# Kernel optimization log

Hardware: AMD Instinct MI355X
Metric: run time of the kernel (lower is better)

The kernel has to match this reference:

```python
import jax, jax.numpy as jnp
import numpy as np

BATCH, DIN, DSTATE, SEQLEN = 4, 2048, 16, 2048


def setup_inputs() -> dict:
    key = jax.random.key(0)
    ks = jax.random.split(key, 7)
    u = jax.random.normal(ks[0], (BATCH, DIN, SEQLEN), dtype=jnp.float32)
    # delta pre-softplus; moderate positive-ish values like Mamba dt_proj output
    delta = jax.random.uniform(ks[1], (BATCH, DIN, SEQLEN), dtype=jnp.float32, minval=-2.0, maxval=1.0)
    # A is negative in real Mamba (A = -exp(A_log)); keep recurrence stable
    A = -jnp.exp(jax.random.uniform(ks[2], (DIN, DSTATE), dtype=jnp.float32, minval=-1.0, maxval=1.0))
    B = jax.random.normal(ks[3], (BATCH, DSTATE, SEQLEN), dtype=jnp.float32)
    C = jax.random.normal(ks[4], (BATCH, DSTATE, SEQLEN), dtype=jnp.float32)
    D = jax.random.normal(ks[5], (DIN,), dtype=jnp.float32)
    z = jax.random.normal(ks[6], (BATCH, DIN, SEQLEN), dtype=jnp.float32)
    return {"u": u, "delta": delta, "A": A, "B": B, "C": C, "D": D, "z": z}


def reference(u, delta, A, B, C, D, z):
    """Mamba selective scan (selective_scan_ref semantics, delta_softplus=True).

    u, delta, z: (b, d, l); A: (d, n); B, C: (b, n, l); D: (d,).
    y_t = C_t . x_t + D*u_t, x_t = exp(dt_t*A)*x_{t-1} + dt_t*B_t*u_t,
    final y gated by SiLU(z).
    """
    dt = jax.nn.softplus(delta)                      # (b, d, l)

    def step(x, inp):
        dt_t, u_t, B_t, C_t = inp                    # (b,d) (b,d) (b,n) (b,n)
        dA = jnp.exp(dt_t[..., None] * A)            # (b, d, n)
        x = x * dA + (dt_t * u_t)[..., None] * B_t[:, None, :]
        y_t = jnp.einsum('bdn,bn->bd', x, C_t)
        return x, y_t

    xs = (jnp.moveaxis(dt, -1, 0),                   # (l, b, d)
          jnp.moveaxis(u, -1, 0),
          jnp.moveaxis(B, -1, 0),                    # (l, b, n)
          jnp.moveaxis(C, -1, 0))
    x0 = jnp.zeros((u.shape[0], u.shape[1], A.shape[1]), dtype=u.dtype)
    _, ys = jax.lax.scan(step, x0, xs)               # ys: (l, b, d)
    y = jnp.moveaxis(ys, 0, -1)                      # (b, d, l)
    y = y + D[None, :, None] * u
    y = y * (z * jax.nn.sigmoid(z))                  # SiLU gate
    return y
```

## Files before the change

### kernel.cpp

```cpp
#include <hip/hip_runtime.h>


#define BATCHSZ 4
#define DIN 2048
#define NSTATE 16
#define SEQ 2048
#define NCH (BATCHSZ * DIN)
#define TT 32
#define L2E 1.44269504f

__device__ __forceinline__ float softplus_f(float v) {
    float e = __builtin_amdgcn_exp2f(v * L2E);
    return 0.69314718f * __builtin_amdgcn_logf(1.0f + e);
}

__device__ __forceinline__ float silu_f(float v) {
    float s = __builtin_amdgcn_rcpf(1.0f + __builtin_amdgcn_exp2f(-v * L2E));
    return v * s;
}

__device__ __forceinline__ float comp4(const float4& f, int k) {
    return k == 0 ? f.x : k == 1 ? f.y : k == 2 ? f.z : f.w;
}

__device__ __forceinline__ void set4(float4& f, int k, float v) {
    if (k == 0) f.x = v; else if (k == 1) f.y = v; else if (k == 2) f.z = v; else f.w = v;
}


template<int NC>
__global__ __launch_bounds__(256, 3) void k_pass1(
        const float* __restrict__ u, const float* __restrict__ delta,
        const float* __restrict__ A, const float* __restrict__ Bm,
        float* __restrict__ ws) {
    constexpr int LC = SEQ / NC;
    constexpr int DB = DIN / 256;
    int blk = blockIdx.x;
    int b = (blk / DB) % BATCHSZ;
    int c = blk / (DB * BATCHSZ);
    int d = (blk % DB) * 256 + threadIdx.x;
    int bd = b * DIN + d;

    float A2[NSTATE];
    const float* Ar = A + d * NSTATE;
    #pragma unroll
    for (int n = 0; n < NSTATE; ++n) A2[n] = Ar[n] * L2E;

    float x[NSTATE];
    #pragma unroll
    for (int n = 0; n < NSTATE; ++n) x[n] = 0.0f;
    float S = 0.0f;

    size_t base = (size_t)bd * SEQ + (size_t)c * LC;
    const float4* u4 = (const float4*)(u + base);
    const float4* d4 = (const float4*)(delta + base);
    const float* Bp = Bm + (size_t)b * NSTATE * SEQ + (size_t)c * LC;

    for (int tile = 0; tile < LC / TT; ++tile) {
        float4 ub[8], db[8];
        #pragma unroll
        for (int j = 0; j < 8; ++j) { ub[j] = u4[tile * 8 + j]; db[j] = d4[tile * 8 + j]; }
        #pragma unroll
        for (int j = 0; j < 8; ++j) {
            #pragma unroll
            for (int k = 0; k < 4; ++k) {
                float dt = softplus_f(comp4(db[j], k));
                S += dt;
                float du = dt * comp4(ub[j], k);
                int t = tile * TT + j * 4 + k;
                #pragma unroll
                for (int n = 0; n < NSTATE; ++n) {
                    float dA = __builtin_amdgcn_exp2f(A2[n] * dt);
                    x[n] = x[n] * dA + du * Bp[n * SEQ + t];
                }
            }
        }
    }
    float* wsq = ws;
    float* wsS = ws + (size_t)NSTATE * NC * NCH;
    #pragma unroll
    for (int n = 0; n < NSTATE; ++n) wsq[((size_t)n * NC + c) * NCH + bd] = x[n];
    wsS[(size_t)c * NCH + bd] = S;
}

template<int NC>
__global__ __launch_bounds__(256) void k_pass2(
        const float* __restrict__ A, float* __restrict__ ws) {
    int bd = blockIdx.x * 256 + threadIdx.x;
    int d = bd & (DIN - 1);

    float A2[NSTATE];
    const float* Ar = A + d * NSTATE;
    #pragma unroll
    for (int n = 0; n < NSTATE; ++n) A2[n] = Ar[n] * L2E;

    float x[NSTATE];
    #pragma unroll
    for (int n = 0; n < NSTATE; ++n) x[n] = 0.0f;

    float* wsq = ws;
    float* wsS = ws + (size_t)NSTATE * NC * NCH;

    for (int c = 0; c < NC; ++c) {
        float S = wsS[(size_t)c * NCH + bd];
        #pragma unroll
        for (int n = 0; n < NSTATE; ++n) {
            float* p = wsq + ((size_t)n * NC + c) * NCH + bd;
            float q = *p;
            float P = __builtin_amdgcn_exp2f(A2[n] * S);
            *p = x[n];
            x[n] = x[n] * P + q;
        }
    }
}

template<int NC>
__global__ __launch_bounds__(256, 3) void k_pass3(
        const float* __restrict__ u, const float* __restrict__ delta,
        const float* __restrict__ A, const float* __restrict__ Bm,
        const float* __restrict__ Cm, const float* __restrict__ Dv,
        const float* __restrict__ z, const float* __restrict__ ws,
        float* __restrict__ out) {
    constexpr int LC = SEQ / NC;
    constexpr int DB = DIN / 256;
    int blk = blockIdx.x;
    int b = (blk / DB) % BATCHSZ;
    int c = blk / (DB * BATCHSZ);
    int d = (blk % DB) * 256 + threadIdx.x;
    int bd = b * DIN + d;

    float A2[NSTATE];
    const float* Ar = A + d * NSTATE;
    #pragma unroll
    for (int n = 0; n < NSTATE; ++n) A2[n] = Ar[n] * L2E;

    const float* wsq = ws;
    float x[NSTATE];
    #pragma unroll
    for (int n = 0; n < NSTATE; ++n)
        x[n] = wsq[((size_t)n * NC + c) * NCH + bd];

    float Dd = Dv[d];
    size_t base = (size_t)bd * SEQ + (size_t)c * LC;
    const float4* u4 = (const float4*)(u + base);
    const float4* d4 = (const float4*)(delta + base);
    const float4* z4 = (const float4*)(z + base);
    float4* o4 = (float4*)(out + base);
    const float* Bp = Bm + (size_t)b * NSTATE * SEQ + (size_t)c * LC;
    const float* Cp = Cm + (size_t)b * NSTATE * SEQ + (size_t)c * LC;

    for (int tile = 0; tile < LC / TT; ++tile) {
        float4 ub[8], db[8];
        #pragma unroll
        for (int j = 0; j < 8; ++j) { ub[j] = u4[tile * 8 + j]; db[j] = d4[tile * 8 + j]; }
        float4 yy[8];
        #pragma unroll
        for (int j = 0; j < 8; ++j) {
            #pragma unroll
            for (int k = 0; k < 4; ++k) {
                float uv = comp4(ub[j], k);
                float dt = softplus_f(comp4(db[j], k));
                float du = dt * uv;
                int t = tile * TT + j * 4 + k;
                float acc = 0.0f;
                #pragma unroll
                for (int n = 0; n < NSTATE; ++n) {
                    float dA = __builtin_amdgcn_exp2f(A2[n] * dt);
                    x[n] = x[n] * dA + du * Bp[n * SEQ + t];
                    acc += x[n] * Cp[n * SEQ + t];
                }
                set4(yy[j], k, acc + Dd * uv);
            }
        }
        float4 zb[8];
        #pragma unroll
        for (int j = 0; j < 8; ++j) zb[j] = z4[tile * 8 + j];
        #pragma unroll
        for (int j = 0; j < 8; ++j) {
            float4 oo;
            #pragma unroll
            for (int k = 0; k < 4; ++k)
                set4(oo, k, comp4(yy[j], k) * silu_f(comp4(zb[j], k)));
            o4[tile * 8 + j] = oo;
        }
    }
}

__global__ __launch_bounds__(256) void k_simple(
        const float* __restrict__ u, const float* __restrict__ delta,
        const float* __restrict__ A, const float* __restrict__ Bm,
        const float* __restrict__ Cm, const float* __restrict__ Dv,
        const float* __restrict__ z, float* __restrict__ out) {
    int bd = blockIdx.x * 256 + threadIdx.x;
    int b  = bd >> 11;
    int d  = bd & (DIN - 1);

    float A2[NSTATE];
    const float* Ar = A + d * NSTATE;
    #pragma unroll
    for (int n = 0; n < NSTATE; ++n) A2[n] = Ar[n] * L2E;
    float x[NSTATE];
    #pragma unroll
    for (int n = 0; n < NSTATE; ++n) x[n] = 0.0f;

    float Dd = Dv[d];
    size_t base = (size_t)bd * SEQ;
    const float4* u4 = (const float4*)(u + base);
    const float4* d4 = (const float4*)(delta + base);
    const float4* z4 = (const float4*)(z + base);
    float4* o4 = (float4*)(out + base);
    const float* Bp = Bm + (size_t)b * NSTATE * SEQ;
    const float* Cp = Cm + (size_t)b * NSTATE * SEQ;

    for (int t4 = 0; t4 < SEQ / 4; ++t4) {
        float4 uu = u4[t4];
        float4 dd = d4[t4];
        float4 zz = z4[t4];
        float4 yy;
        #pragma unroll
        for (int k = 0; k < 4; ++k) {
            float uv = comp4(uu, k);
            float dt = softplus_f(comp4(dd, k));
            float du = dt * uv;
            int t = t4 * 4 + k;
            float acc = 0.0f;
            #pragma unroll
            for (int n = 0; n < NSTATE; ++n) {
                float dA = __builtin_amdgcn_exp2f(A2[n] * dt);
                x[n] = x[n] * dA + du * Bp[n * SEQ + t];
                acc += x[n] * Cp[n * SEQ + t];
            }
            float y = acc + Dd * uv;
            y = y * silu_f(comp4(zz, k));
            set4(yy, k, y);
        }
        o4[t4] = yy;
    }
}

template<int NC>
static void launch_chunked(const float* u, const float* delta, const float* A,
                           const float* Bm, const float* Cm, const float* Dv,
                           const float* z, float* ws, float* out, hipStream_t stream) {
    k_pass1<NC><<<NCH * NC / 256, 256, 0, stream>>>(u, delta, A, Bm, ws);
    k_pass2<NC><<<NCH / 256, 256, 0, stream>>>(A, ws);
    k_pass3<NC><<<NCH * NC / 256, 256, 0, stream>>>(u, delta, A, Bm, Cm, Dv, z, ws, out);
}

extern "C" void kernel_launch(void* const* d_in, const int* in_sizes, int n_in,
                              void* d_out, int out_size, void* d_ws, size_t ws_size,
                              hipStream_t stream) {
    const float* u     = (const float*)d_in[0];
    const float* delta = (const float*)d_in[1];
    const float* A     = (const float*)d_in[2];
    const float* Bm    = (const float*)d_in[3];
    const float* Cm    = (const float*)d_in[4];
    const float* Dv    = (const float*)d_in[5];
    const float* z     = (const float*)d_in[6];
    float* out = (float*)d_out;
    float* ws = (float*)d_ws;

    size_t need32 = (size_t)(NSTATE + 1) * 32 * NCH * sizeof(float);
    size_t need16 = (size_t)(NSTATE + 1) * 16 * NCH * sizeof(float);
    if (ws_size >= need32) {
        launch_chunked<32>(u, delta, A, Bm, Cm, Dv, z, ws, out, stream);
    } else if (ws_size >= need16) {
        launch_chunked<16>(u, delta, A, Bm, Cm, Dv, z, ws, out, stream);
    } else {
        k_simple<<<NCH / 256, 256, 0, stream>>>(u, delta, A, Bm, Cm, Dv, z, out);
    }
}
```

Measured before the change: 459.9 us.

## Stage u/delta and B/C through LDS with coalesced loads, parallelize pass2 per state

Pass1 and pass3 now load u and delta tiles cooperatively with coalesced float4 reads into padded shared memory, prefetching the next tile into registers. The per-chunk B and C slices are transposed into shared memory so each timestep reads 16 states as four float4 LDS loads. Pass3 also writes y back through LDS so z reads and output stores are coalesced. Pass2 gets one thread per (state, channel) for more parallelism, and a 64-chunk variant is added when the workspace allows it. The cost is more shared memory, extra barriers, and lower occupancy.

```diff
diff --git a/kernel.cpp b/kernel.cpp
--- a/kernel.cpp
+++ b/kernel.cpp
@@ -6,7 +6,9 @@
 #define NSTATE 16
 #define SEQ 2048
 #define NCH (BATCHSZ * DIN)
-#define TT 32
+#define NGRP (NCH / 256)
+#define TT 16
+#define ST 20
 #define L2E 1.44269504f
 
 __device__ __forceinline__ float softplus_f(float v) {
@@ -34,48 +36,92 @@
         const float* __restrict__ A, const float* __restrict__ Bm,
         float* __restrict__ ws) {
     constexpr int LC = SEQ / NC;
-    constexpr int DB = DIN / 256;
-    int blk = blockIdx.x;
-    int b = (blk / DB) % BATCHSZ;
-    int c = blk / (DB * BATCHSZ);
-    int d = (blk % DB) * 256 + threadIdx.x;
-    int bd = b * DIN + d;
+    constexpr int NT = LC / TT;
+    __shared__ float Ub[256 * ST];
+    __shared__ float Db[256 * ST];
+    __shared__ float Bc[LC * 20];
+
+    int tid = threadIdx.x;
+    int g = blockIdx.x & (NGRP - 1);
+    int c = blockIdx.x >> 5;
+    int chBase = g << 8;
+    int b = chBase >> 11;
+    int bd = chBase + tid;
+    int d = bd & (DIN - 1);
 
     float A2[NSTATE];
-    const float* Ar = A + d * NSTATE;
-    #pragma unroll
-    for (int n = 0; n < NSTATE; ++n) A2[n] = Ar[n] * L2E;
+    {
+        const float* Ar = A + (size_t)d * NSTATE;
+        #pragma unroll
+        for (int n = 0; n < NSTATE; ++n) A2[n] = Ar[n] * L2E;
+    }
+
+    const float* ug = u + (size_t)chBase * SEQ + (size_t)c * LC;
+    const float* dg = delta + (size_t)chBase * SEQ + (size_t)c * LC;
+    const float* Bg = Bm + (size_t)b * NSTATE * SEQ + (size_t)c * LC;
+
+    #pragma unroll
+    for (int i = 0; i < LC * NSTATE / 256; ++i) {
+        int e = i * 256 + tid;
+        int n = e / LC;
+        int t = e % LC;
+        Bc[t * 20 + n] = Bg[(size_t)n * SEQ + t];
+    }
 
     float x[NSTATE];
     #pragma unroll
     for (int n = 0; n < NSTATE; ++n) x[n] = 0.0f;
     float S = 0.0f;
 
-    size_t base = (size_t)bd * SEQ + (size_t)c * LC;
-    const float4* u4 = (const float4*)(u + base);
-    const float4* d4 = (const float4*)(delta + base);
-    const float* Bp = Bm + (size_t)b * NSTATE * SEQ + (size_t)c * LC;
-
-    for (int tile = 0; tile < LC / TT; ++tile) {
-        float4 ub[8], db[8];
-        #pragma unroll
-        for (int j = 0; j < 8; ++j) { ub[j] = u4[tile * 8 + j]; db[j] = d4[tile * 8 + j]; }
-        #pragma unroll
-        for (int j = 0; j < 8; ++j) {
+    float4 uvr[4], dvr[4];
+    #pragma unroll
+    for (int it = 0; it < 4; ++it) {
+        int r = it * 64 + (tid >> 2), cq = (tid & 3) * 4;
+        uvr[it] = *(const float4*)(ug + (size_t)r * SEQ + cq);
+        dvr[it] = *(const float4*)(dg + (size_t)r * SEQ + cq);
+    }
+
+    for (int tile = 0; tile < NT; ++tile) {
+        int tb = tile * TT;
+        __syncthreads();
+        #pragma unroll
+        for (int it = 0; it < 4; ++it) {
+            int r = it * 64 + (tid >> 2), cq = (tid & 3) * 4;
+            *(float4*)(&Ub[r * ST + cq]) = uvr[it];
+            *(float4*)(&Db[r * ST + cq]) = dvr[it];
+        }
+        __syncthreads();
+        if (tile + 1 < NT) {
+            #pragma unroll
+            for (int it = 0; it < 4; ++it) {
+                int r = it * 64 + (tid >> 2), cq = (tid & 3) * 4;
+                uvr[it] = *(const float4*)(ug + (size_t)r * SEQ + tb + TT + cq);
+                dvr[it] = *(const float4*)(dg + (size_t)r * SEQ + tb + TT + cq);
+            }
+        }
+        #pragma unroll
+        for (int t4 = 0; t4 < TT / 4; ++t4) {
+            float4 u4 = *(const float4*)(&Ub[tid * ST + t4 * 4]);
+            float4 d4 = *(const float4*)(&Db[tid * ST + t4 * 4]);
             #pragma unroll
             for (int k = 0; k < 4; ++k) {
-                float dt = softplus_f(comp4(db[j], k));
+                float dt = softplus_f(comp4(d4, k));
                 S += dt;
-                float du = dt * comp4(ub[j], k);
-                int t = tile * TT + j * 4 + k;
+                float du = dt * comp4(u4, k);
+                int t = tb + t4 * 4 + k;
+                const float4* Br = (const float4*)(&Bc[t * 20]);
+                float bb[NSTATE];
+                *(float4*)&bb[0] = Br[0]; *(float4*)&bb[4] = Br[1];
+                *(float4*)&bb[8] = Br[2]; *(float4*)&bb[12] = Br[3];
                 #pragma unroll
                 for (int n = 0; n < NSTATE; ++n) {
                     float dA = __builtin_amdgcn_exp2f(A2[n] * dt);
-                    x[n] = x[n] * dA + du * Bp[n * SEQ + t];
+                    x[n] = x[n] * dA + du * bb[n];
                 }
             }
         }
     }
+
     float* wsq = ws;
     float* wsS = ws + (size_t)NSTATE * NC * NCH;
     #pragma unroll
@@ -86,31 +132,23 @@
 template<int NC>
 __global__ __launch_bounds__(256) void k_pass2(
         const float* __restrict__ A, float* __restrict__ ws) {
-    int bd = blockIdx.x * 256 + threadIdx.x;
+    int idx = blockIdx.x * 256 + threadIdx.x;
+    int n = idx >> 13;
+    int bd = idx & (NCH - 1);
     int d = bd & (DIN - 1);
 
-    float A2[NSTATE];
-    const float* Ar = A + d * NSTATE;
-    #pragma unroll
-    for (int n = 0; n < NSTATE; ++n) A2[n] = Ar[n] * L2E;
-
-    float x[NSTATE];
-    #pragma unroll
-    for (int n = 0; n < NSTATE; ++n) x[n] = 0.0f;
-
+    float A2 = A[(size_t)d * NSTATE + n] * L2E;
+    float x = 0.0f;
     float* wsq = ws;
     float* wsS = ws + (size_t)NSTATE * NC * NCH;
 
     for (int c = 0; c < NC; ++c) {
         float S = wsS[(size_t)c * NCH + bd];
-        #pragma unroll
-        for (int n = 0; n < NSTATE; ++n) {
-            float* p = wsq + ((size_t)n * NC + c) * NCH + bd;
-            float q = *p;
-            float P = __builtin_amdgcn_exp2f(A2[n] * S);
-            *p = x[n];
-            x[n] = x[n] * P + q;
-        }
+        float* p = wsq + ((size_t)n * NC + c) * NCH + bd;
+        float q = *p;
+        float P = __builtin_amdgcn_exp2f(A2 * S);
+        *p = x;
+        x = x * P + q;
     }
 }
 
@@ -122,66 +160,116 @@
         const float* __restrict__ z, const float* __restrict__ ws,
         float* __restrict__ out) {
     constexpr int LC = SEQ / NC;
-    constexpr int DB = DIN / 256;
-    int blk = blockIdx.x;
-    int b = (blk / DB) % BATCHSZ;
-    int c = blk / (DB * BATCHSZ);
-    int d = (blk % DB) * 256 + threadIdx.x;
-    int bd = b * DIN + d;
+    constexpr int NT = LC / TT;
+    __shared__ float Ub[256 * ST];
+    __shared__ float Db[256 * ST];
+    __shared__ float Bc[LC * 20];
+    __shared__ float Cc[LC * 20];
+
+    int tid = threadIdx.x;
+    int g = blockIdx.x & (NGRP - 1);
+    int c = blockIdx.x >> 5;
+    int chBase = g << 8;
+    int b = chBase >> 11;
+    int bd = chBase + tid;
+    int d = bd & (DIN - 1);
 
     float A2[NSTATE];
-    const float* Ar = A + d * NSTATE;
-    #pragma unroll
-    for (int n = 0; n < NSTATE; ++n) A2[n] = Ar[n] * L2E;
+    {
+        const float* Ar = A + (size_t)d * NSTATE;
+        #pragma unroll
+        for (int n = 0; n < NSTATE; ++n) A2[n] = Ar[n] * L2E;
+    }
+
+    const float* ug = u + (size_t)chBase * SEQ + (size_t)c * LC;
+    const float* dg = delta + (size_t)chBase * SEQ + (size_t)c * LC;
+    const float* zg = z + (size_t)chBase * SEQ + (size_t)c * LC;
+    float* og = out + (size_t)chBase * SEQ + (size_t)c * LC;
+    const float* Bg = Bm + (size_t)b * NSTATE * SEQ + (size_t)c * LC;
+    const float* Cg = Cm + (size_t)b * NSTATE * SEQ + (size_t)c * LC;
+
+    #pragma unroll
+    for (int i = 0; i < LC * NSTATE / 256; ++i) {
+        int e = i * 256 + tid;
+        int n = e / LC;
+        int t = e % LC;
+        Bc[t * 20 + n] = Bg[(size_t)n * SEQ + t];
+        Cc[t * 20 + n] = Cg[(size_t)n * SEQ + t];
+    }
 
     const float* wsq = ws;
     float x[NSTATE];
     #pragma unroll
     for (int n = 0; n < NSTATE; ++n)
         x[n] = wsq[((size_t)n * NC + c) * NCH + bd];
-
     float Dd = Dv[d];
-    size_t base = (size_t)bd * SEQ + (size_t)c * LC;
-    const float4* u4 = (const float4*)(u + base);
-    const float4* d4 = (const float4*)(delta + base);
-    const float4* z4 = (const float4*)(z + base);
-    float4* o4 = (float4*)(out + base);
-    const float* Bp = Bm + (size_t)b * NSTATE * SEQ + (size_t)c * LC;
-    const float* Cp = Cm + (size_t)b * NSTATE * SEQ + (size_t)c * LC;
-
-    for (int tile = 0; tile < LC / TT; ++tile) {
-        float4 ub[8], db[8];
-        #pragma unroll
-        for (int j = 0; j < 8; ++j) { ub[j] = u4[tile * 8 + j]; db[j] = d4[tile * 8 + j]; }
-        float4 yy[8];
-        #pragma unroll
-        for (int j = 0; j < 8; ++j) {
+
+    float4 uvr[4], dvr[4];
+    #pragma unroll
+    for (int it = 0; it < 4; ++it) {
+        int r = it * 64 + (tid >> 2), cq = (tid & 3) * 4;
+        uvr[it] = *(const float4*)(ug + (size_t)r * SEQ + cq);
+        dvr[it] = *(const float4*)(dg + (size_t)r * SEQ + cq);
+    }
+
+    for (int tile = 0; tile < NT; ++tile) {
+        int tb = tile * TT;
+        __syncthreads();
+        #pragma unroll
+        for (int it = 0; it < 4; ++it) {
+            int r = it * 64 + (tid >> 2), cq = (tid & 3) * 4;
+            *(float4*)(&Ub[r * ST + cq]) = uvr[it];
+            *(float4*)(&Db[r * ST + cq]) = dvr[it];
+        }
+        __syncthreads();
+        if (tile + 1 < NT) {
+            #pragma unroll
+            for (int it = 0; it < 4; ++it) {
+                int r = it * 64 + (tid >> 2), cq = (tid & 3) * 4;
+                uvr[it] = *(const float4*)(ug + (size_t)r * SEQ + tb + TT + cq);
+                dvr[it] = *(const float4*)(dg + (size_t)r * SEQ + tb + TT + cq);
+            }
+        }
+        #pragma unroll
+        for (int t4 = 0; t4 < TT / 4; ++t4) {
+            float4 u4 = *(const float4*)(&Ub[tid * ST + t4 * 4]);
+            float4 d4 = *(const float4*)(&Db[tid * ST + t4 * 4]);
+            float4 y4;
             #pragma unroll
             for (int k = 0; k < 4; ++k) {
-                float uv = comp4(ub[j], k);
-                float dt = softplus_f(comp4(db[j], k));
+                float uv = comp4(u4, k);
+                float dt = softplus_f(comp4(d4, k));
                 float du = dt * uv;
-                int t = tile * TT + j * 4 + k;
+                int t = tb + t4 * 4 + k;
+                const float4* Br = (const float4*)(&Bc[t * 20]);
+                const float4* Cr = (const float4*)(&Cc[t * 20]);
+                float bb[NSTATE], cc[NSTATE];
+                *(float4*)&bb[0] = Br[0]; *(float4*)&bb[4] = Br[1];
+                *(float4*)&bb[8] = Br[2]; *(float4*)&bb[12] = Br[3];
+                *(float4*)&cc[0] = Cr[0]; *(float4*)&cc[4] = Cr[1];
+                *(float4*)&cc[8] = Cr[2]; *(float4*)&cc[12] = Cr[3];
                 float acc = 0.0f;
                 #pragma unroll
                 for (int n = 0; n < NSTATE; ++n) {
                     float dA = __builtin_amdgcn_exp2f(A2[n] * dt);
-                    x[n] = x[n] * dA + du * Bp[n * SEQ + t];
-                    acc += x[n] * Cp[n * SEQ + t];
+                    x[n] = x[n] * dA + du * bb[n];
+                    acc += x[n] * cc[n];
                 }
-                set4(yy[j], k, acc + Dd * uv);
-            }
-        }
-        float4 zb[8];
-        #pragma unroll
-        for (int j = 0; j < 8; ++j) zb[j] = z4[tile * 8 + j];
-        #pragma unroll
-        for (int j = 0; j < 8; ++j) {
+                set4(y4, k, acc + Dd * uv);
+            }
+            *(float4*)(&Ub[tid * ST + t4 * 4]) = y4;
+        }
+        __syncthreads();
+        #pragma unroll
+        for (int it = 0; it < 4; ++it) {
+            int r = it * 64 + (tid >> 2), cq = (tid & 3) * 4;
+            float4 y4 = *(const float4*)(&Ub[r * ST + cq]);
+            float4 z4 = *(const float4*)(zg + (size_t)r * SEQ + tb + cq);
             float4 oo;
             #pragma unroll
             for (int k = 0; k < 4; ++k)
-                set4(oo, k, comp4(yy[j], k) * silu_f(comp4(zb[j], k)));
-            o4[tile * 8 + j] = oo;
+                set4(oo, k, comp4(y4, k) * silu_f(comp4(z4, k)));
+            *(float4*)(og + (size_t)r * SEQ + tb + cq) = oo;
         }
     }
 }
@@ -242,9 +330,9 @@
 static void launch_chunked(const float* u, const float* delta, const float* A,
                            const float* Bm, const float* Cm, const float* Dv,
                            const float* z, float* ws, float* out, hipStream_t stream) {
-    k_pass1<NC><<<NCH * NC / 256, 256, 0, stream>>>(u, delta, A, Bm, ws);
-    k_pass2<NC><<<NCH / 256, 256, 0, stream>>>(A, ws);
-    k_pass3<NC><<<NCH * NC / 256, 256, 0, stream>>>(u, delta, A, Bm, Cm, Dv, z, ws, out);
+    k_pass1<NC><<<NGRP * NC, 256, 0, stream>>>(u, delta, A, Bm, ws);
+    k_pass2<NC><<<(NSTATE * NCH) / 256, 256, 0, stream>>>(A, ws);
+    k_pass3<NC><<<NGRP * NC, 256, 0, stream>>>(u, delta, A, Bm, Cm, Dv, z, ws, out);
 }
 
 extern "C" void kernel_launch(void* const* d_in, const int* in_sizes, int n_in,
@@ -260,9 +348,12 @@
     float* out = (float*)d_out;
     float* ws = (float*)d_ws;
 
+    size_t need64 = (size_t)(NSTATE + 1) * 64 * NCH * sizeof(float);
     size_t need32 = (size_t)(NSTATE + 1) * 32 * NCH * sizeof(float);
     size_t need16 = (size_t)(NSTATE + 1) * 16 * NCH * sizeof(float);
-    if (ws_size >= need32) {
+    if (ws_size >= need64) {
+        launch_chunked<64>(u, delta, A, Bm, Cm, Dv, z, ws, out, stream);
+    } else if (ws_size >= need32) {
         launch_chunked<32>(u, delta, A, Bm, Cm, Dv, z, ws, out, stream);
     } else if (ws_size >= need16) {
         launch_chunked<16>(u, delta, A, Bm, Cm, Dv, z, ws, out, stream);
```

Result: faster. 445.0 us (-3.3%).

## Restructure chunked scan into windowed segments with LDS-staged B/C and per-state pass2

Applied to the files above, without the earlier changes.

Rework the three-pass chunked scan so each block covers 32 channels across a 256-step window, with 8 threads per channel scanning 32-step segments (64 chunks total). B and C for the window are staged in shared memory with padded rows. The carry pass is parallelised over both channel and state index, with vectorised, prefetched workspace access. This exposes more parallelism in the sequential carry pass and shortens per-thread dependency chains. In exchange it needs roughly twice the workspace, and if the workspace is too small it falls back to the slow single-pass kernel.

```diff
diff --git a/kernel.cpp b/kernel.cpp
--- a/kernel.cpp
+++ b/kernel.cpp
@@ -6,8 +6,18 @@
 #define NSTATE 16
 #define SEQ 2048
 #define NCH (BATCHSZ * DIN)
-#define TT 32
+#define CHG 32
+#define SEGS 8
+#define SLEN 32
+#define WIN 256
+#define NWIN 8
+#define NCP 64
+#define NG2 256
 #define L2E 1.44269504f
+
+#define WSQ_N 524288
+#define WSQ_T 65536
+#define WSS_OFF 8388608
 
 __device__ __forceinline__ float softplus_f(float v) {
     float e = __builtin_amdgcn_exp2f(v * L2E);
@@ -27,162 +37,208 @@
     if (k == 0) f.x = v; else if (k == 1) f.y = v; else if (k == 2) f.z = v; else f.w = v;
 }
 
-
-template<int NC>
 __global__ __launch_bounds__(256, 3) void k_pass1(
         const float* __restrict__ u, const float* __restrict__ delta,
         const float* __restrict__ A, const float* __restrict__ Bm,
         float* __restrict__ ws) {
-    constexpr int LC = SEQ / NC;
-    constexpr int DB = DIN / 256;
-    int blk = blockIdx.x;
-    int b = (blk / DB) % BATCHSZ;
-    int c = blk / (DB * BATCHSZ);
-    int d = (blk % DB) * 256 + threadIdx.x;
-    int bd = b * DIN + d;
+    __shared__ float Bc[WIN * 20];
+
+    int tid = threadIdx.x;
+    int g = blockIdx.x & (NG2 - 1);
+    int tau = blockIdx.x >> 8;
+    int ch = tid >> 3, seg = tid & 7;
+    int bd = g * CHG + ch;
+    int d = bd & (DIN - 1);
+    int b = bd >> 11;
+
+    const float* up = u + (size_t)bd * SEQ + tau * WIN + seg * SLEN;
+    const float* dp = delta + (size_t)bd * SEQ + tau * WIN + seg * SLEN;
+    float4 uv[8], dv[8];
+    #pragma unroll
+    for (int j = 0; j < 8; ++j) { uv[j] = ((const float4*)up)[j]; dv[j] = ((const float4*)dp)[j]; }
+
+    const float* Bg = Bm + (size_t)b * NSTATE * SEQ + tau * WIN;
+    #pragma unroll
+    for (int m = 0; m < 4; ++m) {
+        float4 v;
+        v.x = Bg[(size_t)(m * 4 + 0) * SEQ + tid];
+        v.y = Bg[(size_t)(m * 4 + 1) * SEQ + tid];
+        v.z = Bg[(size_t)(m * 4 + 2) * SEQ + tid];
+        v.w = Bg[(size_t)(m * 4 + 3) * SEQ + tid];
+        *(float4*)(&Bc[tid * 20 + m * 4]) = v;
+    }
 
     float A2[NSTATE];
-    const float* Ar = A + d * NSTATE;
+    const float* Ar = A + (size_t)d * NSTATE;
     #pragma unroll
     for (int n = 0; n < NSTATE; ++n) A2[n] = Ar[n] * L2E;
+
+    __syncthreads();
 
     float x[NSTATE];
     #pragma unroll
     for (int n = 0; n < NSTATE; ++n) x[n] = 0.0f;
     float S = 0.0f;
 
-    size_t base = (size_t)bd * SEQ + (size_t)c * LC;
-    const float4* u4 = (const float4*)(u + base);
-    const float4* d4 = (const float4*)(delta + base);
-    const float* Bp = Bm + (size_t)b * NSTATE * SEQ + (size_t)c * LC;
-
-    for (int tile = 0; tile < LC / TT; ++tile) {
-        float4 ub[8], db[8];
-        #pragma unroll
-        for (int j = 0; j < 8; ++j) { ub[j] = u4[tile * 8 + j]; db[j] = d4[tile * 8 + j]; }
-        #pragma unroll
-        for (int j = 0; j < 8; ++j) {
+    #pragma unroll
+    for (int j = 0; j < 8; ++j) {
+        #pragma unroll
+        for (int k = 0; k < 4; ++k) {
+            float dt = softplus_f(comp4(dv[j], k));
+            S += dt;
+            float du = dt * comp4(uv[j], k);
+            int tl = seg * SLEN + j * 4 + k;
+            const float4* Br = (const float4*)(&Bc[tl * 20]);
+            float bb[NSTATE];
+            *(float4*)&bb[0] = Br[0]; *(float4*)&bb[4] = Br[1];
+            *(float4*)&bb[8] = Br[2]; *(float4*)&bb[12] = Br[3];
             #pragma unroll
-            for (int k = 0; k < 4; ++k) {
-                float dt = softplus_f(comp4(db[j], k));
-                S += dt;
-                float du = dt * comp4(ub[j], k);
-                int t = tile * TT + j * 4 + k;
-                #pragma unroll
-                for (int n = 0; n < NSTATE; ++n) {
-                    float dA = __builtin_amdgcn_exp2f(A2[n] * dt);
-                    x[n] = x[n] * dA + du * Bp[n * SEQ + t];
-                }
+            for (int n = 0; n < NSTATE; ++n) {
+                float dA = __builtin_amdgcn_exp2f(A2[n] * dt);
+                x[n] = x[n] * dA + du * bb[n];
             }
         }
     }
-    float* wsq = ws;
-    float* wsS = ws + (size_t)NSTATE * NC * NCH;
-    #pragma unroll
-    for (int n = 0; n < NSTATE; ++n) wsq[((size_t)n * NC + c) * NCH + bd] = x[n];
-    wsS[(size_t)c * NCH + bd] = S;
-}
-
-template<int NC>
+
+    size_t qb = (size_t)tau * WSQ_T + (size_t)g * 256 + ch * 8 + seg;
+    #pragma unroll
+    for (int n = 0; n < NSTATE; ++n) ws[(size_t)n * WSQ_N + qb] = x[n];
+    ws[WSS_OFF + qb] = S;
+}
+
 __global__ __launch_bounds__(256) void k_pass2(
         const float* __restrict__ A, float* __restrict__ ws) {
-    int bd = blockIdx.x * 256 + threadIdx.x;
+    int idx = blockIdx.x * 256 + threadIdx.x;
+    int n = idx >> 13;
+    int bd = idx & (NCH - 1);
+    int g = bd >> 5, ch = bd & 31;
     int d = bd & (DIN - 1);
 
-    float A2[NSTATE];
-    const float* Ar = A + d * NSTATE;
-    #pragma unroll
-    for (int n = 0; n < NSTATE; ++n) A2[n] = Ar[n] * L2E;
-
-    float x[NSTATE];
-    #pragma unroll
-    for (int n = 0; n < NSTATE; ++n) x[n] = 0.0f;
-
-    float* wsq = ws;
-    float* wsS = ws + (size_t)NSTATE * NC * NCH;
-
-    for (int c = 0; c < NC; ++c) {
-        float S = wsS[(size_t)c * NCH + bd];
-        #pragma unroll
-        for (int n = 0; n < NSTATE; ++n) {
-            float* p = wsq + ((size_t)n * NC + c) * NCH + bd;
-            float q = *p;
-            float P = __builtin_amdgcn_exp2f(A2[n] * S);
-            *p = x[n];
-            x[n] = x[n] * P + q;
-        }
-    }
-}
-
-template<int NC>
+    float A2 = A[(size_t)d * NSTATE + n] * L2E;
+
+    size_t qb = (size_t)n * WSQ_N + (size_t)g * 256 + ch * 8;
+    size_t sb = WSS_OFF + (size_t)g * 256 + ch * 8;
+
+    float x = 0.0f;
+    float4 Sa = *(const float4*)(ws + sb);
+    float4 Sb = *(const float4*)(ws + sb + 4);
+    float4 qa = *(const float4*)(ws + qb);
+    float4 q2 = *(const float4*)(ws + qb + 4);
+
+    #pragma unroll
+    for (int tau = 0; tau < NWIN; ++tau) {
+        float4 nSa, nSb, nqa, nq2;
+        if (tau + 1 < NWIN) {
+            nSa = *(const float4*)(ws + sb + (size_t)(tau + 1) * WSQ_T);
+            nSb = *(const float4*)(ws + sb + (size_t)(tau + 1) * WSQ_T + 4);
+            nqa = *(const float4*)(ws + qb + (size_t)(tau + 1) * WSQ_T);
+            nq2 = *(const float4*)(ws + qb + (size_t)(tau + 1) * WSQ_T + 4);
+        }
+        float Sv[8], qv[8], xs[8];
+        *(float4*)&Sv[0] = Sa; *(float4*)&Sv[4] = Sb;
+        *(float4*)&qv[0] = qa; *(float4*)&qv[4] = q2;
+        #pragma unroll
+        for (int s = 0; s < 8; ++s) {
+            xs[s] = x;
+            x = x * __builtin_amdgcn_exp2f(A2 * Sv[s]) + qv[s];
+        }
+        *(float4*)(ws + qb + (size_t)tau * WSQ_T) = *(float4*)&xs[0];
+        *(float4*)(ws + qb + (size_t)tau * WSQ_T + 4) = *(float4*)&xs[4];
+        Sa = nSa; Sb = nSb; qa = nqa; q2 = nq2;
+    }
+}
+
 __global__ __launch_bounds__(256, 3) void k_pass3(
         const float* __restrict__ u, const float* __restrict__ delta,
         const float* __restrict__ A, const float* __restrict__ Bm,
         const float* __restrict__ Cm, const float* __restrict__ Dv,
         const float* __restrict__ z, const float* __restrict__ ws,
         float* __restrict__ out) {
-    constexpr int LC = SEQ / NC;
-    constexpr int DB = DIN / 256;
-    int blk = blockIdx.x;
-    int b = (blk / DB) % BATCHSZ;
-    int c = blk / (DB * BATCHSZ);
-    int d = (blk % DB) * 256 + threadIdx.x;
-    int bd = b * DIN + d;
+    __shared__ float Bc[WIN * 20];
+    __shared__ float Cc[WIN * 20];
+
+    int tid = threadIdx.x;
+    int g = blockIdx.x & (NG2 - 1);
+    int tau = blockIdx.x >> 8;
+    int ch = tid >> 3, seg = tid & 7;
+    int bd = g * CHG + ch;
+    int d = bd & (DIN - 1);
+    int b = bd >> 11;
+
+    size_t qb = (size_t)tau * WSQ_T + (size_t)g * 256 + ch * 8 + seg;
+    float x[NSTATE];
+    #pragma unroll
+    for (int n = 0; n < NSTATE; ++n) x[n] = ws[(size_t)n * WSQ_N + qb];
+
+    const float* up = u + (size_t)bd * SEQ + tau * WIN + seg * SLEN;
+    const float* dp = delta + (size_t)bd * SEQ + tau * WIN + seg * SLEN;
+    float4 uv[8], dv[8];
+    #pragma unroll
+    for (int j = 0; j < 8; ++j) { uv[j] = ((const float4*)up)[j]; dv[j] = ((const float4*)dp)[j]; }
+
+    const float* Bg = Bm + (size_t)b * NSTATE * SEQ + tau * WIN;
+    const float* Cg = Cm + (size_t)b * NSTATE * SEQ + tau * WIN;
+    #pragma unroll
+    for (int m = 0; m < 4; ++m) {
+        float4 v, w;
+        v.x = Bg[(size_t)(m * 4 + 0) * SEQ + tid];
+        v.y = Bg[(size_t)(m * 4 + 1) * SEQ + tid];
+        v.z = Bg[(size_t)(m * 4 + 2) * SEQ + tid];
+        v.w = Bg[(size_t)(m * 4 + 3) * SEQ + tid];
+        w.x = Cg[(size_t)(m * 4 + 0) * SEQ + tid];
+        w.y = Cg[(size_t)(m * 4 + 1) * SEQ + tid];
+        w.z = Cg[(size_t)(m * 4 + 2) * SEQ + tid];
+        w.w = Cg[(size_t)(m * 4 + 3) * SEQ + tid];
+        *(float4*)(&Bc[tid * 20 + m * 4]) = v;
+        *(float4*)(&Cc[tid * 20 + m * 4]) = w;
+    }
 
     float A2[NSTATE];
-    const float* Ar = A + d * NSTATE;
+    const float* Ar = A + (size_t)d * NSTATE;
     #pragma unroll
     for (int n = 0; n < NSTATE; ++n) A2[n] = Ar[n] * L2E;
-
-    const float* wsq = ws;
-    float x[NSTATE];
-    #pragma unroll
-    for (int n = 0; n < NSTATE; ++n)
-        x[n] = wsq[((size_t)n * NC + c) * NCH + bd];
-
     float Dd = Dv[d];
-    size_t base = (size_t)bd * SEQ + (size_t)c * LC;
-    const float4* u4 = (const float4*)(u + base);
-    const float4* d4 = (const float4*)(delta + base);
-    const float4* z4 = (const float4*)(z + base);
-    float4* o4 = (float4*)(out + base);
-    const float* Bp = Bm + (size_t)b * NSTATE * SEQ + (size_t)c * LC;
-    const float* Cp = Cm + (size_t)b * NSTATE * SEQ + (size_t)c * LC;
-
-    for (int tile = 0; tile < LC / TT; ++tile) {
-        float4 ub[8], db[8];
-        #pragma unroll
-        for (int j = 0; j < 8; ++j) { ub[j] = u4[tile * 8 + j]; db[j] = d4[tile * 8 + j]; }
-        float4 yy[8];
-        #pragma unroll
-        for (int j = 0; j < 8; ++j) {
+
+    __syncthreads();
+
+    #pragma unroll
+    for (int j = 0; j < 8; ++j) {
+        #pragma unroll
+        for (int k = 0; k < 4; ++k) {
+            float uvk = comp4(uv[j], k);
+            float dt = softplus_f(comp4(dv[j], k));
+            float du = dt * uvk;
+            int tl = seg * SLEN + j * 4 + k;
+            const float4* Br = (const float4*)(&Bc[tl * 20]);
+            const float4* Cr = (const float4*)(&Cc[tl * 20]);
+            float bb[NSTATE], cc[NSTATE];
+            *(float4*)&bb[0] = Br[0]; *(float4*)&bb[4] = Br[1];
+            *(float4*)&bb[8] = Br[2]; *(float4*)&bb[12] = Br[3];
+            *(float4*)&cc[0] = Cr[0]; *(float4*)&cc[4] = Cr[1];
+            *(float4*)&cc[8] = Cr[2]; *(float4*)&cc[12] = Cr[3];
+            float acc = 0.0f;
             #pragma unroll
-            for (int k = 0; k < 4; ++k) {
-                float uv = comp4(ub[j], k);
-                float dt = softplus_f(comp4(db[j], k));
-                float du = dt * uv;
-                int t = tile * TT + j * 4 + k;
-                float acc = 0.0f;
-                #pragma unroll
-                for (int n = 0; n < NSTATE; ++n) {
-                    float dA = __builtin_amdgcn_exp2f(A2[n] * dt);
-                    x[n] = x[n] * dA + du * Bp[n * SEQ + t];
-                    acc += x[n] * Cp[n * SEQ + t];
-                }
-                set4(yy[j], k, acc + Dd * uv);
+            for (int n = 0; n < NSTATE; ++n) {
+                float dA = __builtin_amdgcn_exp2f(A2[n] * dt);
+                x[n] = x[n] * dA + du * bb[n];
+                acc += x[n] * cc[n];
             }
-        }
-        float4 zb[8];
-        #pragma unroll
-        for (int j = 0; j < 8; ++j) zb[j] = z4[tile * 8 + j];
-        #pragma unroll
-        for (int j = 0; j < 8; ++j) {
-            float4 oo;
-            #pragma unroll
-            for (int k = 0; k < 4; ++k)
-                set4(oo, k, comp4(yy[j], k) * silu_f(comp4(zb[j], k)));
-            o4[tile * 8 + j] = oo;
-        }
+            set4(uv[j], k, acc + Dd * uvk);
+        }
+    }
+
+    const float* zp = z + (size_t)bd * SEQ + tau * WIN + seg * SLEN;
+    float* op = out + (size_t)bd * SEQ + tau * WIN + seg * SLEN;
+    float4 zv[8];
+    #pragma unroll
+    for (int j = 0; j < 8; ++j) zv[j] = ((const float4*)zp)[j];
+    #pragma unroll
+    for (int j = 0; j < 8; ++j) {
+        float4 oo;
+        #pragma unroll
+        for (int k = 0; k < 4; ++k)
+            set4(oo, k, comp4(uv[j], k) * silu_f(comp4(zv[j], k)));
+        ((float4*)op)[j] = oo;
     }
 }
 
@@ -219,9 +275,9 @@
         float4 yy;
         #pragma unroll
         for (int k = 0; k < 4; ++k) {
-            float uv = comp4(uu, k);
+            float uvk = comp4(uu, k);
             float dt = softplus_f(comp4(dd, k));
-            float du = dt * uv;
+            float du = dt * uvk;
             int t = t4 * 4 + k;
             float acc = 0.0f;
             #pragma unroll
@@ -230,21 +286,12 @@
                 x[n] = x[n] * dA + du * Bp[n * SEQ + t];
                 acc += x[n] * Cp[n * SEQ + t];
             }
-            float y = acc + Dd * uv;
+            float y = acc + Dd * uvk;
             y = y * silu_f(comp4(zz, k));
             set4(yy, k, y);
         }
         o4[t4] = yy;
     }
-}
-
-template<int NC>
-static void launch_chunked(const float* u, const float* delta, const float* A,
-                           const float* Bm, const float* Cm, const float* Dv,
-                           const float* z, float* ws, float* out, hipStream_t stream) {
-    k_pass1<NC><<<NCH * NC / 256, 256, 0, stream>>>(u, delta, A, Bm, ws);
-    k_pass2<NC><<<NCH / 256, 256, 0, stream>>>(A, ws);
-    k_pass3<NC><<<NCH * NC / 256, 256, 0, stream>>>(u, delta, A, Bm, Cm, Dv, z, ws, out);
 }
 
 extern "C" void kernel_launch(void* const* d_in, const int* in_sizes, int n_in,
@@ -260,12 +307,11 @@
     float* out = (float*)d_out;
     float* ws = (float*)d_ws;
 
-    size_t need32 = (size_t)(NSTATE + 1) * 32 * NCH * sizeof(float);
-    size_t need16 = (size_t)(NSTATE + 1) * 16 * NCH * sizeof(float);
-    if (ws_size >= need32) {
-        launch_chunked<32>(u, delta, A, Bm, Cm, Dv, z, ws, out, stream);
-    } else if (ws_size >= need16) {
-        launch_chunked<16>(u, delta, A, Bm, Cm, Dv, z, ws, out, stream);
+    size_t need = (size_t)(NSTATE + 1) * NCP * NCH * sizeof(float);
+    if (ws_size >= need) {
+        k_pass1<<<NWIN * NG2, 256, 0, stream>>>(u, delta, A, Bm, ws);
+        k_pass2<<<(NSTATE * NCH) / 256, 256, 0, stream>>>(A, ws);
+        k_pass3<<<NWIN * NG2, 256, 0, stream>>>(u, delta, A, Bm, Cm, Dv, z, ws, out);
     } else {
         k_simple<<<NCH / 256, 256, 0, stream>>>(u, delta, A, Bm, Cm, Dv, z, out);
     }
```

Measured after the change: 977.3 us. 112% more time.
